# Kernel optimization log

Hardware: AMD Instinct MI355X
Metric: run time of the kernel (lower is better)

## Reference

```python
import jax, jax.numpy as jnp
import numpy as np
import math

N_HEADS = 16
ROPE_BASE = 10000.0


def rotate_half(x):
    x1 = x[..., ::2]
    x2 = x[..., 1::2]
    return jnp.stack((-x2, x1), axis=-1).reshape(x.shape)


def rope_tables(seq_len, head_dim, dtype):
    inv_freq = 1.0 / (ROPE_BASE ** (jnp.arange(0, head_dim, 2, dtype=jnp.float32) / head_dim))
    positions = jnp.arange(seq_len, dtype=jnp.float32)
    freqs = jnp.outer(positions, inv_freq)            # [S, hd/2]
    emb = jnp.concatenate((freqs, freqs), axis=-1)    # [S, hd]  (matches torch cat convention)
    cos = jnp.cos(emb)[None, None, :, :].astype(dtype)
    sin = jnp.sin(emb)[None, None, :, :].astype(dtype)
    return cos, sin


def setup_inputs() -> dict:
    key = jax.random.key(0)
    k1, k2, k3 = jax.random.split(key, 3)
    B, S, D = 2, 2048, 1024
    x = jax.random.normal(k1, (B, S, D), dtype=jnp.float32)
    # causal lower-triangular mask, broadcastable over batch and heads
    mask = jnp.tril(jnp.ones((S, S), dtype=jnp.int32))[None, None, :, :]
    w_qkv = jax.random.normal(k2, (D, 3 * D), dtype=jnp.float32) * 0.02
    w_out = jax.random.normal(k3, (D, D), dtype=jnp.float32) * 0.02
    return {"x": x, "mask": mask, "w_qkv": w_qkv, "w_out": w_out}


def reference(x, mask, w_qkv, w_out):
    B, S, D = x.shape
    H = N_HEADS
    hd = D // H
    qkv = (x @ w_qkv).reshape(B, S, 3, H, hd)
    qkv = jnp.transpose(qkv, (2, 0, 3, 1, 4))         # [3, B, H, S, hd]
    q, k, v = qkv[0], qkv[1], qkv[2]
    cos, sin = rope_tables(S, hd, x.dtype)
    q = q * cos + rotate_half(q) * sin
    k = k * cos + rotate_half(k) * sin
    scale = math.sqrt(hd)
    attn = jnp.einsum("bhsd,bhtd->bhst", q, k) / scale
    attn = jnp.where(mask == 0, -jnp.inf, attn)
    attn = jax.nn.softmax(attn, axis=-1)              # dropout p=0.0 -> identity
    out = jnp.einsum("bhst,bhtd->bhsd", attn, v)
    out = jnp.transpose(out, (0, 2, 1, 3)).reshape(B, S, D)
    return out @ w_out
```

## Files before the change

kernel.cpp:

```cpp
#include <hip/hip_runtime.h>
#include <stdint.h>

typedef unsigned short u16;
typedef __bf16 bf16x8 __attribute__((ext_vector_type(8)));
typedef float f32x4 __attribute__((ext_vector_type(4)));

#define S_LEN 2048
#define NH    16
#define DM    1024
#define N3    3072
#define MROWS 4096

__device__ __forceinline__ float b2f(u16 u) {
  unsigned int v = ((unsigned int)u) << 16;
  return __builtin_bit_cast(float, v);
}
__device__ __forceinline__ u16 f2b(float f) {
  unsigned int v = __builtin_bit_cast(unsigned int, f);
  v += 0x7fffu + ((v >> 16) & 1u);
  return (u16)(v >> 16);
}
__device__ __forceinline__ u16 f2b_trunc(float f) {
  return (u16)(__builtin_bit_cast(unsigned int, f) >> 16);
}
__device__ __forceinline__ bf16x8 ld8(const u16* p) { return *(const bf16x8*)p; }
__device__ __forceinline__ f32x4 mfma16(bf16x8 a, bf16x8 b, f32x4 c) {
  return __builtin_amdgcn_mfma_f32_16x16x32_bf16(a, b, c, 0, 0, 0);
}
__device__ __forceinline__ void glds16(const void* g, void* l) {
  __builtin_amdgcn_global_load_lds(
      (const __attribute__((address_space(1))) unsigned int*)g,
      (__attribute__((address_space(3))) unsigned int*)l, 16, 0, 0);
}
__device__ __forceinline__ int bfish(unsigned int w) {
  unsigned int e = (w >> 7) & 0xffu;
  return (e >= 100u && e <= 134u) ? 1 : 0;
}

__global__ __launch_bounds__(256) void prep_kernel(const void* __restrict__ x,
                                                   const void* __restrict__ wqkv,
                                                   const void* __restrict__ wout,
                                                   u16* __restrict__ xb,
                                                   u16* __restrict__ wqT,
                                                   u16* __restrict__ woT,
                                                   float* __restrict__ cs,
                                                   int* __restrict__ flag) {
  const int bx = blockIdx.x;
  const int t = threadIdx.x;
  if (bx < 2048) {
    __shared__ int cnt;
    if (t == 0) cnt = 0;
    __syncthreads();
    size_t i = (size_t)bx * 256 + t;
    const uint4* xv = (const uint4*)x;
    uint4 probe = xv[i];
    unsigned int wds[4]; *(uint4*)wds = probe;
    atomicAdd(&cnt, bfish(wds[0]) + bfish(wds[1]) + bfish(wds[2]) + bfish(wds[3]));
    __syncthreads();
    const int isbf = cnt > 512;
    if (t == 0) *flag = isbf;
    if (isbf) {
      ((uint4*)xb)[i] = probe;
    } else {
      const float* xf = (const float*)x;
      #pragma unroll
      for (int j = 0; j < 8; ++j) xb[i * 8 + j] = f2b(xf[i * 8 + j]);
    }
    return;
  }
  if (bx < 2560) {
    int i = (bx - 2048) * 256 + t;
    int d = i >> 11, s = i & 2047;
    int f = d & 31;
    float invf = expf(-(float)(2 * f) * (1.0f / 64.0f) * logf(10000.0f));
    float th = (float)s * invf;
    float sv, cv;
    sincosf(th, &sv, &cv);
    cs[i * 2] = cv; cs[i * 2 + 1] = sv;
    return;
  }
  const int wq = bx < 3328;
  const int id = wq ? (bx - 2560) : (bx - 3328);
  const int ncx = wq ? 48 : 16;
  const void* in = wq ? wqkv : wout;
  u16* out = wq ? wqT : woT;
  const int C = wq ? 3072 : 1024;
  const int c0 = (id % ncx) * 64, r0 = (id / ncx) * 64;
  __shared__ int cnt;
  __shared__ u16 L[4096];
  if (t == 0) cnt = 0;
  __syncthreads();
  const unsigned int* wv = (const unsigned int*)in;
  size_t off = (((size_t)id) * 256 + t) & 262143;
  atomicAdd(&cnt, bfish(wv[off]));
  __syncthreads();
  const int fl = cnt > 128;
  if (fl) {
    #pragma unroll
    for (int it = 0; it < 2; ++it) {
      int c = it * 256 + t;
      int rl = c >> 3, cseg = c & 7;
      uint4 v = *(const uint4*)((const u16*)in + (size_t)(r0 + rl) * C + c0 + cseg * 8);
      u16 e[8]; *(uint4*)e = v;
      #pragma unroll
      for (int jj = 0; jj < 8; ++jj) {
        int cl = cseg * 8 + jj;
        L[cl * 64 + (rl ^ (cseg << 3))] = e[jj];
      }
    }
  } else {
    const float* inf_ = (const float*)in;
    #pragma unroll
    for (int it = 0; it < 16; ++it) {
      int c = it * 256 + t;
      int rl = c >> 6, cl = c & 63;
      L[cl * 64 + (rl ^ ((cl >> 3) << 3))] = f2b(inf_[(size_t)(r0 + rl) * C + c0 + cl]);
    }
  }
  __syncthreads();
  #pragma unroll
  for (int it = 0; it < 2; ++it) {
    int c = it * 256 + t;
    int cl = c >> 3, rseg = c & 7;
    uint4 v = *(const uint4*)(L + cl * 64 + (((rseg ^ (cl >> 3)) & 7) << 3));
    *(uint4*)(out + (size_t)(c0 + cl) * 1024 + r0 + rseg * 8) = v;
  }
}

__global__ __launch_bounds__(256) void gemm_qkv(const u16* __restrict__ A,
                                                const u16* __restrict__ Bt,
                                                u16* __restrict__ Qo,
                                                u16* __restrict__ Ko,
                                                u16* __restrict__ Vt,
                                                const float* __restrict__ cs) {
  __shared__ u16 smem[16384];
  u16* Al = smem;
  u16* Bl = smem + 8192;
  const int t = threadIdx.x;
  const int lane = t & 63, wave = t >> 6;
  const int ln = lane & 15, quad = lane >> 4;
  const int wr = wave >> 1, wc = wave & 1;
  const int m0 = blockIdx.x * 128, n0 = blockIdx.y * 128;
  const char* Ab = (const char*)A;
  const char* Bb = (const char*)Bt;
  f32x4 acc[4][4] = {};

  for (int k0 = 0; k0 < 1024; k0 += 64) {
    __syncthreads();
    #pragma unroll
    for (int it = 0; it < 4; ++it) {
      int c = it * 256 + t;
      int row = c >> 3;
      int sg = (c & 7) ^ (row & 7);
      glds16(Ab + ((size_t)(m0 + row) * 1024 + k0 + sg * 8) * 2, (char*)Al + c * 16);
      glds16(Bb + ((size_t)(n0 + row) * 1024 + k0 + sg * 8) * 2, (char*)Bl + c * 16);
    }
    __syncthreads();
    bf16x8 a[4][2], b[4][2];
    #pragma unroll
    for (int i = 0; i < 4; ++i) {
      const int row = wr * 64 + i * 16 + ln;
      #pragma unroll
      for (int ki = 0; ki < 2; ++ki)
        a[i][ki] = ld8(Al + row * 64 + (((ki * 4 + quad) ^ (row & 7)) << 3));
    }
    #pragma unroll
    for (int j = 0; j < 4; ++j) {
      const int row = wc * 64 + j * 16 + ln;
      #pragma unroll
      for (int ki = 0; ki < 2; ++ki)
        b[j][ki] = ld8(Bl + row * 64 + (((ki * 4 + quad) ^ (row & 7)) << 3));
    }
    #pragma unroll
    for (int i = 0; i < 4; ++i)
      #pragma unroll
      for (int j = 0; j < 4; ++j) {
        acc[i][j] = mfma16(a[i][0], b[j][0], acc[i][j]);
        acc[i][j] = mfma16(a[i][1], b[j][1], acc[i][j]);
      }
  }

  const int which = n0 >> 10;
  if (which < 2) {
    u16* dst = which ? Ko : Qo;
    const float qs = which ? 1.0f : 0.18033688011112042f;
    #pragma unroll
    for (int i = 0; i < 4; ++i) {
      const int mb = m0 + wr * 64 + i * 16 + quad * 4;
      const int s0 = mb & 2047, b_ = mb >> 11;
      #pragma unroll
      for (int j = 0; j < 4; ++j) {
        const int c = n0 + wc * 64 + j * 16 + ln;
        const int h = (c >> 6) & 15, d = c & 63;
        const float sgn = (d & 1) ? 1.0f : -1.0f;
        const float4* csp = (const float4*)(cs + ((size_t)d * 2048 + s0) * 2);
        const float4 c01 = csp[0], c23 = csp[1];
        const float cosv[4] = {c01.x, c01.z, c23.x, c23.z};
        const float sinv[4] = {c01.y, c01.w, c23.y, c23.w};
        u16* drow = dst + ((size_t)(b_ * NH + h) * S_LEN + s0) * 64 + d;
        #pragma unroll
        for (int r = 0; r < 4; ++r) {
          const float v = acc[i][j][r];
          const float p = __shfl_xor(v, 1);
          drow[r * 64] = f2b((v * cosv[r] + sgn * p * sinv[r]) * qs);
        }
      }
    }
  } else {
    #pragma unroll
    for (int i = 0; i < 4; ++i)
      #pragma unroll
      for (int j = 0; j < 4; ++j) {
        const int c = n0 + wc * 64 + j * 16 + ln;
        const int h = (c >> 6) & 15, d = c & 63;
        const int m = m0 + wr * 64 + i * 16 + quad * 4;
        const int s = m & 2047, b_ = m >> 11;
        u16 pk[4];
        #pragma unroll
        for (int r = 0; r < 4; ++r) pk[r] = f2b(acc[i][j][r]);
        *(uint2*)&Vt[((size_t)(b_ * NH + h) * 64 + d) * S_LEN + s] = *(const uint2*)pk;
      }
  }
}

__global__ __launch_bounds__(256) void attn_kernel(const u16* __restrict__ Qb,
                                                   const u16* __restrict__ Kb,
                                                   const u16* __restrict__ Vt,
                                                   u16* __restrict__ Ao) {
  __shared__ u16 smem[20480];
  u16* Kl = smem;
  u16* Vl = smem + 8192;
  u16* Pl = smem + 16384;
  const int t = threadIdx.x;
  const int lane = t & 63, w = t >> 6;
  const int ln = lane & 15, quad = lane >> 4;
  const int i = blockIdx.x;
  const int xcd = i & 7;
  const int j = i >> 3;
  const int bh = (xcd << 2) | (j & 3);
  const int q5 = j >> 2;
  const int g = q5 & 7, s5 = q5 >> 3;
  const int qt = (s5 & 1) ? (31 - ((s5 >> 1) << 3) - g) : (((s5 >> 1) << 3) + g);
  const int q0 = qt * 64;
  const int b = bh >> 4, h = bh & 15;
  const u16* Qbh = Qb + (size_t)bh * (S_LEN * 64);
  const u16* Kbh = Kb + (size_t)bh * (S_LEN * 64);
  const u16* Vtbh = Vt + (size_t)bh * (64 * S_LEN);
  u16* Plw = Pl + w * 1024;
  u16* AoBase = Ao + (size_t)b * S_LEN * DM + h * 64;

  auto stage = [&](int kt, int bufi) {
    u16* kd = Kl + bufi * 4096;
    u16* vd = Vl + bufi * 4096;
    const u16* kg = Kbh + (size_t)kt * 64 * 64;
    const u16* vg = Vtbh + (size_t)kt * 64;
    #pragma unroll
    for (int it = 0; it < 2; ++it) {
      int c = it * 256 + t;
      int row = c >> 3, sg = (c & 7) ^ (row & 7);
      glds16((const char*)kg + ((size_t)row * 64 + sg * 8) * 2,   (char*)kd + c * 16);
      glds16((const char*)vg + ((size_t)row * 2048 + sg * 8) * 2, (char*)vd + c * 16);
    }
  };

  bf16x8 bq[2];
  #pragma unroll
  for (int kk = 0; kk < 2; ++kk)
    bq[kk] = ld8(Qbh + (size_t)(q0 + w * 16 + ln) * 64 + kk * 32 + quad * 8);

  f32x4 o[4] = {};
  float l = 0.f;

  stage(0, 0);
  __syncthreads();

  for (int kt = 0; kt <= qt; ++kt) {
    const int bufi = kt & 1;
    if (kt < qt) stage(kt + 1, bufi ^ 1);
    const u16* Kb_ = Kl + bufi * 4096;
    const u16* Vb_ = Vl + bufi * 4096;

    f32x4 st[4] = {};
    #pragma unroll
    for (int kk = 0; kk < 2; ++kk)
      #pragma unroll
      for (int ct = 0; ct < 4; ++ct) {
        bf16x8 ak = ld8(Kb_ + (ct * 16 + ln) * 64 + (((kk * 4 + quad) ^ (ln & 7)) << 3));
        st[ct] = mfma16(ak, bq[kk], st[ct]);
      }

    const bool diag = (kt == qt);
    #pragma unroll
    for (int ct = 0; ct < 4; ++ct) {
      u16 pk[4];
      #pragma unroll
      for (int r = 0; r < 4; ++r) {
        float p;
        if (diag && (ct * 16 + quad * 4 + r) > (w * 16 + ln)) p = 0.f;
        else p = __builtin_amdgcn_exp2f(st[ct][r]);
        l += p;
        pk[r] = f2b_trunc(p);
      }
      *(uint2*)(Plw + ln * 64 + ((((ct * 2) + (quad >> 1)) ^ (ln & 7)) << 3)
                + ((quad & 1) << 2)) = *(const uint2*)pk;
    }

    #pragma unroll
    for (int k4 = 0; k4 < 2; ++k4) {
      bf16x8 bp = ld8(Plw + ln * 64 + (((k4 * 4 + quad) ^ (ln & 7)) << 3));
      #pragma unroll
      for (int dt = 0; dt < 4; ++dt) {
        bf16x8 av = ld8(Vb_ + (dt * 16 + ln) * 64 + (((k4 * 4 + quad) ^ (ln & 7)) << 3));
        o[dt] = mfma16(av, bp, o[dt]);
      }
    }
    __syncthreads();
  }

  l += __shfl_xor(l, 16);
  l += __shfl_xor(l, 32);
  const float inv = 1.f / l;
  const size_t qrow = (size_t)(q0 + w * 16 + ln) * DM;
  #pragma unroll
  for (int dt = 0; dt < 4; ++dt) {
    u16 pk[4];
    #pragma unroll
    for (int r = 0; r < 4; ++r) pk[r] = f2b(o[dt][r] * inv);
    *(uint2*)(AoBase + qrow + dt * 16 + quad * 4) = *(const uint2*)pk;
  }
}

template <int TM>
__global__ __launch_bounds__(256) void gemm_out_t(const u16* __restrict__ A,
                                                  const u16* __restrict__ Bt,
                                                  void* __restrict__ Out,
                                                  const int* __restrict__ flag) {
  constexpr int MI = TM / 32;
  __shared__ u16 smem[(TM + 128) * 32];
  u16* Al = smem;
  u16* Bl = smem + TM * 32;
  const int t = threadIdx.x;
  const int lane = t & 63, wave = t >> 6;
  const int ln = lane & 15, quad = lane >> 4;
  const int wr = wave >> 1, wc = wave & 1;
  const int m0 = blockIdx.x * TM, n0 = blockIdx.y * 128;
  const int rr = t >> 2;
  const int cb = (t & 3) * 16;
  const char* Ab = (const char*)A;
  const char* Bb = (const char*)Bt;
  f32x4 acc[MI][4] = {};

  for (int k0 = 0; k0 < 1024; k0 += 32) {
    __syncthreads();
    #pragma unroll
    for (int p = 0; p < TM / 64; ++p)
      glds16(Ab + ((size_t)(m0 + p * 64 + rr) * 1024 + k0) * 2 + cb,
             (char*)Al + p * 4096 + t * 16);
    glds16(Bb + ((size_t)(n0 + rr) * 1024 + k0) * 2 + cb,      (char*)Bl + t * 16);
    glds16(Bb + ((size_t)(n0 + 64 + rr) * 1024 + k0) * 2 + cb, (char*)Bl + 4096 + t * 16);
    __syncthreads();
    bf16x8 a[MI], b[4];
    #pragma unroll
    for (int i = 0; i < MI; ++i)
      a[i] = ld8(Al + (wr * (TM / 2) + i * 16 + ln) * 32 + quad * 8);
    #pragma unroll
    for (int j = 0; j < 4; ++j)
      b[j] = ld8(Bl + (wc * 64 + j * 16 + ln) * 32 + quad * 8);
    #pragma unroll
    for (int i = 0; i < MI; ++i)
      #pragma unroll
      for (int j = 0; j < 4; ++j)
        acc[i][j] = mfma16(a[i], b[j], acc[i][j]);
  }

  const int fl = *flag;
  #pragma unroll
  for (int i = 0; i < MI; ++i)
    #pragma unroll
    for (int j = 0; j < 4; ++j)
      #pragma unroll
      for (int r = 0; r < 4; ++r) {
        int m = m0 + wr * (TM / 2) + i * 16 + quad * 4 + r;
        int c = n0 + wc * 64 + j * 16 + ln;
        float v = acc[i][j][r];
        if (fl) ((u16*)Out)[(size_t)m * DM + c] = f2b(v);
        else    ((float*)Out)[(size_t)m * DM + c] = v;
      }
}

extern "C" void kernel_launch(void* const* d_in, const int* in_sizes, int n_in,
                              void* d_out, int out_size, void* d_ws, size_t ws_size,
                              hipStream_t stream) {
  (void)in_sizes; (void)n_in; (void)out_size; (void)ws_size;
  const void* x    = d_in[0];
  const void* wqkv = d_in[2];
  const void* wout = d_in[3];
  char* ws = (char*)d_ws;
  u16*  xb   = (u16*)(ws + 0);
  u16*  Ao   = xb;
  u16*  wqT  = (u16*)(ws + 8388608);
  u16*  woT  = (u16*)(ws + 14680064);
  u16*  Qb   = (u16*)(ws + 16777216);
  u16*  Kb   = (u16*)(ws + 25165824);
  u16*  Vt   = (u16*)(ws + 33554432);
  float* cs  = (float*)(ws + 41943040);
  int*  flag = (int*)(ws + 42991616);

  prep_kernel<<<3584, 256, 0, stream>>>(x, wqkv, wout, xb, wqT, woT, cs, flag);
  gemm_qkv<<<dim3(32, 24), 256, 0, stream>>>(xb, wqT, Qb, Kb, Vt, cs);
  attn_kernel<<<1024, 256, 0, stream>>>(Qb, Kb, Vt, Ao);
  gemm_out_t<64><<<dim3(64, 8), 256, 0, stream>>>(Ao, woT, d_out, flag);
}
```

Before: 189.9 us.

## Restructure QKV GEMM into 256x256 tiles with double-buffered LDS pipelining

The QKV projection GEMM moves from 128x128 tiles with 4 waves to 256x256 tiles with 8 waves. It adds a double-buffered LDS pipeline that issues global-to-LDS loads for the next K slices in quarters, interleaved with MFMA phases that use s_setprio and explicit barriers. The goal is to hide global load latency and raise per-block data reuse. The cost is 128KB of LDS per block, more accumulator registers, and a grid of only 192 blocks, which may leave some CUs idle on a 256-CU device.

```diff
diff --git a/kernel.cpp b/kernel.cpp
--- a/kernel.cpp
+++ b/kernel.cpp
@@ -127,57 +127,107 @@
   }
 }
 
-__global__ __launch_bounds__(256) void gemm_qkv(const u16* __restrict__ A,
-                                                const u16* __restrict__ Bt,
-                                                u16* __restrict__ Qo,
-                                                u16* __restrict__ Ko,
-                                                u16* __restrict__ Vt,
-                                                const float* __restrict__ cs) {
-  __shared__ u16 smem[16384];
-  u16* Al = smem;
-  u16* Bl = smem + 8192;
+
+#define PHASE_PRE() do { \
+  asm volatile("" ::: "memory"); \
+  __builtin_amdgcn_s_barrier(); \
+  asm volatile("s_waitcnt lgkmcnt(0)" ::: "memory"); \
+  __builtin_amdgcn_sched_barrier(0); \
+  __builtin_amdgcn_s_setprio(1); \
+} while (0)
+
+#define PHASE_POST() do { \
+  __builtin_amdgcn_s_setprio(0); \
+  asm volatile("" ::: "memory"); \
+  __builtin_amdgcn_s_barrier(); \
+} while (0)
+
+#define LOADA(P) \
+  _Pragma("unroll") \
+  for (int ii = 0; ii < 2; ++ii) { \
+    const int row = wr * 128 + ((P) * 2 + ii) * 16 + ln; \
+    _Pragma("unroll") \
+    for (int kk = 0; kk < 2; ++kk) \
+      a[ii][kk] = ld8(Ap + row * 64 + (((kk * 4 + quad) ^ (row & 7)) << 3)); \
+  }
+
+#define MFMAQ(P) \
+  _Pragma("unroll") \
+  for (int ii = 0; ii < 2; ++ii) { \
+    _Pragma("unroll") \
+    for (int j = 0; j < 4; ++j) { \
+      acc[(P) * 2 + ii][j] = mfma16(a[ii][0], b[j][0], acc[(P) * 2 + ii][j]); \
+      acc[(P) * 2 + ii][j] = mfma16(a[ii][1], b[j][1], acc[(P) * 2 + ii][j]); \
+    } \
+  }
+
+__global__ __launch_bounds__(512, 2) void gemm_qkv(const u16* __restrict__ A,
+                                                   const u16* __restrict__ Bt,
+                                                   u16* __restrict__ Qo,
+                                                   u16* __restrict__ Ko,
+                                                   u16* __restrict__ Vt,
+                                                   const float* __restrict__ cs) {
+  __shared__ u16 smem[2][32768];
   const int t = threadIdx.x;
   const int lane = t & 63, wave = t >> 6;
   const int ln = lane & 15, quad = lane >> 4;
-  const int wr = wave >> 1, wc = wave & 1;
-  const int m0 = blockIdx.x * 128, n0 = blockIdx.y * 128;
-  const char* Ab = (const char*)A;
-  const char* Bb = (const char*)Bt;
-  f32x4 acc[4][4] = {};
-
-  for (int k0 = 0; k0 < 1024; k0 += 64) {
-    __syncthreads();
-    #pragma unroll
-    for (int it = 0; it < 4; ++it) {
-      int c = it * 256 + t;
-      int row = c >> 3;
-      int sg = (c & 7) ^ (row & 7);
-      glds16(Ab + ((size_t)(m0 + row) * 1024 + k0 + sg * 8) * 2, (char*)Al + c * 16);
-      glds16(Bb + ((size_t)(n0 + row) * 1024 + k0 + sg * 8) * 2, (char*)Bl + c * 16);
-    }
-    __syncthreads();
-    bf16x8 a[4][2], b[4][2];
-    #pragma unroll
-    for (int i = 0; i < 4; ++i) {
-      const int row = wr * 64 + i * 16 + ln;
-      #pragma unroll
-      for (int ki = 0; ki < 2; ++ki)
-        a[i][ki] = ld8(Al + row * 64 + (((ki * 4 + quad) ^ (row & 7)) << 3));
-    }
+  const int wr = wave >> 2, wc = wave & 3;
+  const int m0 = blockIdx.x * 256, n0 = blockIdx.y * 256;
+  const u16* gA0 = A + (size_t)m0 * 1024;
+  const u16* gA1 = A + (size_t)(m0 + 128) * 1024;
+  const u16* gB0 = Bt + (size_t)n0 * 1024;
+  const u16* gB1 = Bt + (size_t)(n0 + 128) * 1024;
+  f32x4 acc[8][4] = {};
+
+  auto stage_half = [&](u16* lds, const u16* g, int k0) {
+    #pragma unroll
+    for (int it = 0; it < 2; ++it) {
+      const int c = it * 512 + t;
+      const int row = c >> 3, sg = (c & 7) ^ (row & 7);
+      glds16(g + (size_t)row * 1024 + k0 + sg * 8, (char*)lds + c * 16);
+    }
+  };
+
+  stage_half(&smem[0][0],     gA0, 0);
+  stage_half(&smem[0][8192],  gA1, 0);
+  stage_half(&smem[0][16384], gB0, 0);
+  stage_half(&smem[0][24576], gB1, 0);
+  stage_half(&smem[1][16384], gB0, 64);
+  stage_half(&smem[1][24576], gB1, 64);
+  asm volatile("s_waitcnt vmcnt(4)" ::: "memory");
+  __builtin_amdgcn_s_barrier();
+
+  for (int kt = 0; kt < 16; ++kt) {
+    const int p = kt & 1;
+    u16* Ap = &smem[p][0];
+    u16* Bp = &smem[p][16384];
+    u16* Aq = &smem[p ^ 1][0];
+    const int kA = (kt + 1) * 64, kB = (kt + 2) * 64;
+    bf16x8 b[4][2], a[2][2];
     #pragma unroll
     for (int j = 0; j < 4; ++j) {
       const int row = wc * 64 + j * 16 + ln;
       #pragma unroll
-      for (int ki = 0; ki < 2; ++ki)
-        b[j][ki] = ld8(Bl + row * 64 + (((ki * 4 + quad) ^ (row & 7)) << 3));
-    }
-    #pragma unroll
-    for (int i = 0; i < 4; ++i)
-      #pragma unroll
-      for (int j = 0; j < 4; ++j) {
-        acc[i][j] = mfma16(a[i][0], b[j][0], acc[i][j]);
-        acc[i][j] = mfma16(a[i][1], b[j][1], acc[i][j]);
-      }
+      for (int kk = 0; kk < 2; ++kk)
+        b[j][kk] = ld8(Bp + row * 64 + (((kk * 4 + quad) ^ (row & 7)) << 3));
+    }
+    LOADA(0);
+    if (kt < 15) stage_half(Aq, gA0, kA);
+    PHASE_PRE(); MFMAQ(0); PHASE_POST();
+    LOADA(1);
+    if (kt < 15) stage_half(Aq + 8192, gA1, kA);
+    PHASE_PRE(); MFMAQ(1); PHASE_POST();
+    LOADA(2);
+    if (kt < 14) stage_half(Bp, gB0, kB);
+    PHASE_PRE(); MFMAQ(2); PHASE_POST();
+    LOADA(3);
+    if (kt < 14) stage_half(Bp + 8192, gB1, kB);
+    PHASE_PRE(); MFMAQ(3);
+    __builtin_amdgcn_s_setprio(0);
+    if (kt < 14) { asm volatile("s_waitcnt vmcnt(4)" ::: "memory"); }
+    else         { asm volatile("s_waitcnt vmcnt(0)" ::: "memory"); }
+    asm volatile("" ::: "memory");
+    __builtin_amdgcn_s_barrier();
   }
 
   const int which = n0 >> 10;
@@ -185,13 +235,13 @@
     u16* dst = which ? Ko : Qo;
     const float qs = which ? 1.0f : 0.18033688011112042f;
     #pragma unroll
-    for (int i = 0; i < 4; ++i) {
-      const int mb = m0 + wr * 64 + i * 16 + quad * 4;
+    for (int i = 0; i < 8; ++i) {
+      const int mb = m0 + wr * 128 + i * 16 + quad * 4;
       const int s0 = mb & 2047, b_ = mb >> 11;
       #pragma unroll
       for (int j = 0; j < 4; ++j) {
-        const int c = n0 + wc * 64 + j * 16 + ln;
-        const int h = (c >> 6) & 15, d = c & 63;
+        const int c = (n0 & 1023) + wc * 64 + j * 16 + ln;
+        const int h = c >> 6, d = c & 63;
         const float sgn = (d & 1) ? 1.0f : -1.0f;
         const float4* csp = (const float4*)(cs + ((size_t)d * 2048 + s0) * 2);
         const float4 c01 = csp[0], c23 = csp[1];
@@ -201,27 +251,33 @@
         #pragma unroll
         for (int r = 0; r < 4; ++r) {
           const float v = acc[i][j][r];
-          const float p = __shfl_xor(v, 1);
-          drow[r * 64] = f2b((v * cosv[r] + sgn * p * sinv[r]) * qs);
+          const float pp = __shfl_xor(v, 1);
+          drow[r * 64] = f2b((v * cosv[r] + sgn * pp * sinv[r]) * qs);
         }
       }
     }
   } else {
     #pragma unroll
-    for (int i = 0; i < 4; ++i)
+    for (int i = 0; i < 8; ++i) {
+      const int m = m0 + wr * 128 + i * 16 + quad * 4;
+      const int s = m & 2047, b_ = m >> 11;
       #pragma unroll
       for (int j = 0; j < 4; ++j) {
-        const int c = n0 + wc * 64 + j * 16 + ln;
-        const int h = (c >> 6) & 15, d = c & 63;
-        const int m = m0 + wr * 64 + i * 16 + quad * 4;
-        const int s = m & 2047, b_ = m >> 11;
+        const int c = (n0 & 1023) + wc * 64 + j * 16 + ln;
+        const int h = c >> 6, d = c & 63;
         u16 pk[4];
         #pragma unroll
         for (int r = 0; r < 4; ++r) pk[r] = f2b(acc[i][j][r]);
         *(uint2*)&Vt[((size_t)(b_ * NH + h) * 64 + d) * S_LEN + s] = *(const uint2*)pk;
       }
-  }
-}
+    }
+  }
+}
+
+#undef PHASE_PRE
+#undef PHASE_POST
+#undef LOADA
+#undef MFMAQ
 
 __global__ __launch_bounds__(256) void attn_kernel(const u16* __restrict__ Qb,
                                                    const u16* __restrict__ Kb,
@@ -407,7 +463,7 @@
   int*  flag = (int*)(ws + 42991616);
 
   prep_kernel<<<3584, 256, 0, stream>>>(x, wqkv, wout, xb, wqT, woT, cs, flag);
-  gemm_qkv<<<dim3(32, 24), 256, 0, stream>>>(xb, wqT, Qb, Kb, Vt, cs);
+  gemm_qkv<<<dim3(16, 12), 512, 0, stream>>>(xb, wqT, Qb, Kb, Vt, cs);
   attn_kernel<<<1024, 256, 0, stream>>>(Qb, Kb, Vt, Ao);
   gemm_out_t<64><<<dim3(64, 8), 256, 0, stream>>>(Ao, woT, d_out, flag);
 }
```

After: 186.3 us. About the same (-1.9%).
